# Kernel tuning notes

Measured on AMD Instinct MI355X. Metric: run time of the kernel, lower is better.

Reference implementation:

```python
import jax, jax.numpy as jnp
import numpy as np

B, N, H = 32, 2048, 128


def _lstm_step(c, h, x, Wi, Wh, b):
    # flax LSTMCell: gates i,f,g,o; sigmoid/sigmoid/tanh/sigmoid
    gates = x @ Wi + h @ Wh + b  # (B,N,4H)
    i, f, g, o = jnp.split(gates, 4, axis=-1)
    c_new = jax.nn.sigmoid(f) * c + jax.nn.sigmoid(i) * jnp.tanh(g)
    h_new = jax.nn.sigmoid(o) * jnp.tanh(c_new)
    return c_new, h_new


def setup_inputs() -> dict:
    key = jax.random.key(0)
    ks = jax.random.split(key, 24)
    f32 = jnp.float32
    inp = {}
    inp['node_embeddings'] = jax.random.normal(ks[0], (B, N, H), f32)
    for nm, k in zip(['hs_c0', 'hs_h0', 'hs_c1', 'hs_h1'], ks[1:5]):
        inp[nm] = jax.random.normal(k, (B, N, H), f32)
    ip = jax.random.uniform(ks[5], (B, N), f32)
    inp['instruction_pointer'] = ip / jnp.sum(ip, axis=-1, keepdims=True)
    inp['Wi0'] = jax.random.normal(ks[6], (H, 4 * H), f32) * 0.05
    inp['Wh0'] = jax.random.normal(ks[7], (H, 4 * H), f32) * 0.05
    inp['b0'] = jnp.zeros((4 * H,), f32)
    inp['Wi1'] = jax.random.normal(ks[8], (H, 4 * H), f32) * 0.05
    inp['Wh1'] = jax.random.normal(ks[9], (H, 4 * H), f32) * 0.05
    inp['b1'] = jnp.zeros((4 * H,), f32)
    inp['W_raise'] = jax.random.normal(ks[10], (4 * H, 2), f32) * 0.05
    inp['b_raise'] = jnp.zeros((2,), f32)
    inp['W_branch'] = jax.random.normal(ks[11], (4 * H, 2), f32) * 0.05
    inp['b_branch'] = jnp.zeros((2,), f32)
    inp['true_indexes'] = jax.random.randint(ks[12], (B, N), 0, N, jnp.int32)
    inp['false_indexes'] = jax.random.randint(ks[13], (B, N), 0, N, jnp.int32)
    inp['raise_indexes'] = jax.random.randint(ks[14], (B, N), 0, N, jnp.int32)
    inp['exit_node_indexes'] = jax.random.randint(ks[15], (B,), 0, N, jnp.int32)
    inp['raise_node_indexes'] = jax.random.randint(ks[16], (B,), 0, N, jnp.int32)
    inp['step_limits'] = jax.random.randint(ks[17], (B,), 0, 100, jnp.int32)
    inp['current_step'] = 5
    return inp


def reference(node_embeddings, hs_c0, hs_h0, hs_c1, hs_h1, instruction_pointer,
              Wi0, Wh0, b0, Wi1, Wh1, b1, W_raise, b_raise, W_branch, b_branch,
              true_indexes, false_indexes, raise_indexes,
              exit_node_indexes, raise_node_indexes, step_limits, current_step):
    bidx = jnp.arange(B)
    old = [hs_c0, hs_h0, hs_c1, hs_h1]

    # execute: per-node 2-layer stacked LSTM (vectorized over B,N)
    c0n, h0n = _lstm_step(hs_c0, hs_h0, node_embeddings, Wi0, Wh0, b0)
    c1n, h1n = _lstm_step(hs_c1, hs_h1, h0n, Wi1, Wh1, b1)
    contrib = [c0n, h0n, c1n, h1n]

    # mask_h: keep old state at exit node and (raise_in_ipagnn) at raise node
    def mask_nodes(hc, ho, idx):
        return hc.at[bidx, idx].set(ho[bidx, idx])
    contrib = [mask_nodes(mask_nodes(hc, ho, exit_node_indexes), ho, raise_node_indexes)
               for hc, ho in zip(contrib, old)]

    hs_emb = jnp.concatenate(contrib, axis=-1)  # (B,N,4H)

    raise_dec = jax.nn.softmax(hs_emb @ W_raise + b_raise, axis=-1)
    zero_one = jnp.array([0.0, 1.0], dtype=raise_dec.dtype)
    raise_dec = raise_dec.at[bidx, exit_node_indexes].set(zero_one)
    raise_dec = raise_dec.at[bidx, raise_node_indexes].set(zero_one)
    branch_dec = jax.nn.softmax(hs_emb @ W_branch + b_branch, axis=-1)

    p_raise = raise_dec[..., 0]
    p_noraise = raise_dec[..., 1]
    p_true = p_noraise * branch_dec[..., 0]
    p_false = p_noraise * branch_dec[..., 1]

    seg = jax.vmap(lambda v, idx: jax.ops.segment_sum(v, idx, num_segments=N))
    ip = instruction_pointer
    ip_new = (seg(p_raise * ip, raise_indexes)
              + seg(p_true * ip, true_indexes)
              + seg(p_false * ip, false_indexes))  # (B,N)
    denom = (ip_new + 1e-7)[..., None]

    wr = (p_raise * ip)[..., None]
    wt = (p_true * ip)[..., None]
    wf = (p_false * ip)[..., None]

    def agg(h):
        return (seg(h * wr, raise_indexes) + seg(h * wt, true_indexes)
                + seg(h * wf, false_indexes)) / denom
    hs_new = [agg(h) for h in contrib]

    # keep_old_if_done
    not_done = (current_step < step_limits)  # (B,)
    hs_out = [jnp.where(not_done[:, None, None], hn, ho) for hn, ho in zip(hs_new, old)]
    ip_out = jnp.where(not_done[:, None], ip_new, ip)

    # pack carry: (c0,h0,c1,h1, instruction_pointer) -> (B,N,4H+1)
    return jnp.concatenate(hs_out + [ip_out[..., None]], axis=-1)
```

## Files before the change

### kernel.cpp

```cpp
#include <hip/hip_runtime.h>
#include <stdint.h>

#define BB 32
#define NN 2048
#define HH 128
#define BN (BB*NN)

typedef short v8s __attribute__((ext_vector_type(8)));
typedef float v4f __attribute__((ext_vector_type(4)));

__device__ __forceinline__ unsigned short f2b(float f){
  union { float f; unsigned int i; } v; v.f = f;
  unsigned int x = v.i;
  unsigned int r = x + 0x7FFFu + ((x >> 16) & 1u);
  return (unsigned short)(r >> 16);
}
__device__ __forceinline__ unsigned int pk2(float a, float b){
  return (unsigned int)f2b(a) | ((unsigned int)f2b(b) << 16);
}
__device__ __forceinline__ float b2f(unsigned int s){
  union { unsigned int i; float f; } v; v.i = s << 16; return v.f;
}
__device__ __forceinline__ float frcp(float x){ return __builtin_amdgcn_rcpf(x); }
__device__ __forceinline__ float fsigm(float x){ return frcp(1.0f + __expf(-x)); }
__device__ __forceinline__ float ftanh(float x){ return 1.0f - 2.0f*frcp(1.0f + __expf(2.0f*x)); }

__global__ __launch_bounds__(1024) void kprep(
    const int* __restrict__ ri, const int* __restrict__ ti,
    const int* __restrict__ fi,
    int* __restrict__ counts, int* __restrict__ offsets,
    unsigned short* __restrict__ edges,
    const float* __restrict__ Wi0, const float* __restrict__ Wh0,
    const float* __restrict__ Wi1, const float* __restrict__ Wh1,
    unsigned short* __restrict__ Bsw0, unsigned short* __restrict__ Bsw1)
{
  __shared__ int cnt[NN];
  __shared__ int off[NN];
  __shared__ int cur[NN];
  __shared__ int wpart[16];

  int tid = threadIdx.x;

  if (blockIdx.x >= 32){
    int idx = (blockIdx.x - 32)*1024 + tid;
    int bid = idx >> 6;
    int lane = idx & 63;
    int layer = bid >> 8;
    int kc = (bid >> 5) & 7;
    int ct = bid & 31;
    const float* Wi = layer ? Wi1 : Wi0;
    const float* Wh = layer ? Wh1 : Wh0;
    unsigned short* dst = layer ? Bsw1 : Bsw0;
    int col = ct*16 + (lane & 15);
    int kbase = kc*32 + (lane >> 4)*8;
    size_t o = ((size_t)(kc*32 + ct)*64 + (size_t)lane)*8;
    #pragma unroll
    for (int j = 0; j < 8; j++){
      int k = kbase + j;
      dst[o + j] = f2b((k < 128) ? Wi[k*512 + col] : Wh[(k-128)*512 + col]);
    }
    return;
  }

  int b = blockIdx.x;
  const int* rp = ri + b*NN;
  const int* tp = ti + b*NN;
  const int* fp = fi + b*NN;

  #pragma unroll
  for (int p = 0; p < 2; p++){ cnt[p*1024 + tid] = 0; cur[p*1024 + tid] = 0; }
  __syncthreads();

  int rv[2], tv[2], fv[2];
  #pragma unroll
  for (int p = 0; p < 2; p++){
    int n = p*1024 + tid;
    rv[p] = rp[n]; tv[p] = tp[n]; fv[p] = fp[n];
    atomicAdd(&cnt[rv[p]], 1);
    atomicAdd(&cnt[tv[p]], 1);
    atomicAdd(&cnt[fv[p]], 1);
  }
  __syncthreads();

  int c0 = cnt[2*tid], c1 = cnt[2*tid+1];
  int s = c0 + c1;
  int lane = tid & 63, wv = tid >> 6;
  int inc = s;
  #pragma unroll
  for (int d = 1; d < 64; d <<= 1){
    int t = __shfl_up(inc, d, 64);
    if (lane >= d) inc += t;
  }
  if (lane == 63) wpart[wv] = inc;
  __syncthreads();
  if (tid == 0){
    int run = 0;
    #pragma unroll
    for (int w = 0; w < 16; w++){ int t = wpart[w]; wpart[w] = run; run += t; }
  }
  __syncthreads();
  int excl = wpart[wv] + inc - s;
  off[2*tid]   = excl;
  off[2*tid+1] = excl + c0;
  offsets[b*NN + 2*tid]   = excl;
  offsets[b*NN + 2*tid+1] = excl + c0;
  counts[b*NN + 2*tid]   = c0;
  counts[b*NN + 2*tid+1] = c1;
  __syncthreads();

  size_t ebase = (size_t)b*3*NN;
  #pragma unroll
  for (int p = 0; p < 2; p++){
    int n = p*1024 + tid;
    int t0 = rv[p]; int p0 = atomicAdd(&cur[t0], 1);
    edges[ebase + off[t0] + p0] = (unsigned short)n;
    int t1 = tv[p]; int p1 = atomicAdd(&cur[t1], 1);
    edges[ebase + off[t1] + p1] = (unsigned short)(n | (1<<11));
    int t2 = fv[p]; int p2 = atomicAdd(&cur[t2], 1);
    edges[ebase + off[t2] + p2] = (unsigned short)(n | (2<<11));
  }
}

#define ROWSB 32
#define PA 264
#define PH 136

__global__ __launch_bounds__(512, 4) void klstm2(
    const float* __restrict__ ne,
    float* __restrict__ c0, float* __restrict__ h0,
    float* __restrict__ c1, float* __restrict__ h1,
    unsigned short* __restrict__ sc0, unsigned short* __restrict__ sh0,
    unsigned short* __restrict__ sc1, unsigned short* __restrict__ sh1,
    const unsigned short* __restrict__ Bsw0, const float* __restrict__ b0,
    const unsigned short* __restrict__ Bsw1, const float* __restrict__ b1,
    const int* __restrict__ exit_idx, const int* __restrict__ raise_idx,
    const int* __restrict__ step_limits, const int* __restrict__ cur_step,
    int useb)
{
  __shared__ unsigned short ldsA[ROWSB*PA];
  __shared__ unsigned short ldsH[ROWSB*PH];
  __shared__ unsigned short ldsG[ROWSB*PH];

  int rowbase = blockIdx.x * ROWSB;
  int b = rowbase >> 11;
  if (cur_step[0] >= step_limits[b]) return;

  int tid = threadIdx.x;
  int wid = tid >> 6, lane = tid & 63;
  int quad = lane >> 4, l16 = lane & 15;
  int ch = wid*16 + l16;
  int e_row = exit_idx[b], r_row = raise_idx[b];

  #pragma unroll
  for (int p = 0; p < 4; p++){
    int idx = p*512 + tid;
    int row = idx >> 6, chunk = idx & 63;
    size_t g = (size_t)(rowbase + row)*128 + (chunk & 31)*4;
    float4 v = (chunk < 32) ? *(const float4*)(ne + g) : *(const float4*)(h0 + g);
    uint2 w; w.x = pk2(v.x, v.y); w.y = pk2(v.z, v.w);
    *(uint2*)&ldsA[row*PA + chunk*4] = w;
  }
  __syncthreads();

  float cpre[8], bias[4];
  #pragma unroll
  for (int rt = 0; rt < 2; rt++)
    #pragma unroll
    for (int r = 0; r < 4; r++)
      cpre[rt*4+r] = c0[((size_t)rowbase + rt*16 + quad*4 + r)*128 + ch];
  #pragma unroll
  for (int g = 0; g < 4; g++) bias[g] = b0[g*128 + ch];

  #pragma unroll
  for (int p = 0; p < 2; p++){
    int idx = p*512 + tid;
    int row = idx >> 5, chunk = idx & 31;
    float4 v = *(const float4*)(h1 + (size_t)(rowbase + row)*128 + chunk*4);
    uint2 w; w.x = pk2(v.x, v.y); w.y = pk2(v.z, v.w);
    *(uint2*)&ldsH[row*PH + chunk*4] = w;
  }

  const v8s* Bv0 = (const v8s*)Bsw0;
  v4f acc[2][4] = {};
  v8s bc[4], bn[4];
  #pragma unroll
  for (int g = 0; g < 4; g++) bc[g] = Bv0[(size_t)(g*8 + wid)*64 + lane];
  #pragma unroll
  for (int kc = 0; kc < 8; kc++){
    if (kc < 7){
      #pragma unroll
      for (int g = 0; g < 4; g++) bn[g] = Bv0[(size_t)((kc+1)*32 + g*8 + wid)*64 + lane];
    }
    v8s a0 = *(const v8s*)&ldsA[(0*16 + l16)*PA + kc*32 + quad*8];
    v8s a1 = *(const v8s*)&ldsA[(1*16 + l16)*PA + kc*32 + quad*8];
    #pragma unroll
    for (int g = 0; g < 4; g++){
      acc[0][g] = __builtin_amdgcn_mfma_f32_16x16x32_bf16(a0, bc[g], acc[0][g], 0,0,0);
      acc[1][g] = __builtin_amdgcn_mfma_f32_16x16x32_bf16(a1, bc[g], acc[1][g], 0,0,0);
    }
    #pragma unroll
    for (int g = 0; g < 4; g++) bc[g] = bn[g];
  }

  #pragma unroll
  for (int rt = 0; rt < 2; rt++){
    #pragma unroll
    for (int r = 0; r < 4; r++){
      int k = rt*4 + r;
      int lrow = rt*16 + quad*4 + r;
      int grow = rowbase + lrow;
      int node = grow & 2047;
      bool special = (node == e_row) || (node == r_row);
      float iv = acc[rt][0][r] + bias[0];
      float fv = acc[rt][1][r] + bias[1];
      float gv = acc[rt][2][r] + bias[2];
      float ov = acc[rt][3][r] + bias[3];
      float cn = fsigm(fv)*cpre[k] + fsigm(iv)*ftanh(gv);
      float hn = fsigm(ov)*ftanh(cn);
      if (useb){
        sc0[(size_t)grow*128 + ch] = special ? f2b(cpre[k]) : f2b(cn);
        sh0[(size_t)grow*128 + ch] = special ? ldsA[lrow*PA + 128 + ch] : f2b(hn);
      } else if (!special){
        c0[(size_t)grow*128 + ch] = cn;
        h0[(size_t)grow*128 + ch] = hn;
      }
      ldsG[lrow*PH + ch] = f2b(hn);
    }
  }

  #pragma unroll
  for (int rt = 0; rt < 2; rt++)
    #pragma unroll
    for (int r = 0; r < 4; r++)
      cpre[rt*4+r] = c1[((size_t)rowbase + rt*16 + quad*4 + r)*128 + ch];
  #pragma unroll
  for (int g = 0; g < 4; g++) bias[g] = b1[g*128 + ch];
  const v8s* Bv1 = (const v8s*)Bsw1;
  #pragma unroll
  for (int g = 0; g < 4; g++) bc[g] = Bv1[(size_t)(g*8 + wid)*64 + lane];

  __syncthreads();

  #pragma unroll
  for (int rt = 0; rt < 2; rt++)
    #pragma unroll
    for (int g = 0; g < 4; g++)
      acc[rt][g] = (v4f){0.f, 0.f, 0.f, 0.f};
  #pragma unroll
  for (int kc = 0; kc < 8; kc++){
    if (kc < 7){
      #pragma unroll
      for (int g = 0; g < 4; g++) bn[g] = Bv1[(size_t)((kc+1)*32 + g*8 + wid)*64 + lane];
    }
    v8s a0, a1;
    if (kc < 4){
      a0 = *(const v8s*)&ldsG[(0*16 + l16)*PH + kc*32 + quad*8];
      a1 = *(const v8s*)&ldsG[(1*16 + l16)*PH + kc*32 + quad*8];
    } else {
      a0 = *(const v8s*)&ldsH[(0*16 + l16)*PH + (kc-4)*32 + quad*8];
      a1 = *(const v8s*)&ldsH[(1*16 + l16)*PH + (kc-4)*32 + quad*8];
    }
    #pragma unroll
    for (int g = 0; g < 4; g++){
      acc[0][g] = __builtin_amdgcn_mfma_f32_16x16x32_bf16(a0, bc[g], acc[0][g], 0,0,0);
      acc[1][g] = __builtin_amdgcn_mfma_f32_16x16x32_bf16(a1, bc[g], acc[1][g], 0,0,0);
    }
    #pragma unroll
    for (int g = 0; g < 4; g++) bc[g] = bn[g];
  }

  #pragma unroll
  for (int rt = 0; rt < 2; rt++){
    #pragma unroll
    for (int r = 0; r < 4; r++){
      int k = rt*4 + r;
      int lrow = rt*16 + quad*4 + r;
      int grow = rowbase + lrow;
      int node = grow & 2047;
      bool special = (node == e_row) || (node == r_row);
      float iv = acc[rt][0][r] + bias[0];
      float fv = acc[rt][1][r] + bias[1];
      float gv = acc[rt][2][r] + bias[2];
      float ov = acc[rt][3][r] + bias[3];
      float cn = fsigm(fv)*cpre[k] + fsigm(iv)*ftanh(gv);
      float hn = fsigm(ov)*ftanh(cn);
      if (useb){
        sc1[(size_t)grow*128 + ch] = special ? f2b(cpre[k]) : f2b(cn);
        sh1[(size_t)grow*128 + ch] = special ? ldsH[lrow*PH + ch] : f2b(hn);
      } else if (!special){
        c1[(size_t)grow*128 + ch] = cn;
        h1[(size_t)grow*128 + ch] = hn;
      }
    }
  }
}

__global__ __launch_bounds__(256) void kdec(
    const float* __restrict__ c0, const float* __restrict__ h0,
    const float* __restrict__ c1, const float* __restrict__ h1,
    const unsigned short* __restrict__ sc0, const unsigned short* __restrict__ sh0,
    const unsigned short* __restrict__ sc1, const unsigned short* __restrict__ sh1,
    const float* __restrict__ Wr, const float* __restrict__ br,
    const float* __restrict__ Wb, const float* __restrict__ bb,
    const float* __restrict__ ip,
    const int* __restrict__ exit_idx, const int* __restrict__ raise_idx,
    float* __restrict__ wbuf, int useb)
{
  int tid = threadIdx.x;
  int wid = tid >> 6, lane = tid & 63;
  int gid = blockIdx.x*4 + wid;
  int b = gid >> 11, n = gid & 2047;

  float hv[8];
  if (useb){
    const unsigned short* bufs16[4] = {sc0, sh0, sc1, sh1};
    const unsigned short* hb = bufs16[lane >> 4] + (size_t)gid*128 + (lane & 15)*8;
    uint4 raw = *(const uint4*)hb;
    hv[0] = b2f(raw.x & 0xffffu); hv[1] = b2f(raw.x >> 16);
    hv[2] = b2f(raw.y & 0xffffu); hv[3] = b2f(raw.y >> 16);
    hv[4] = b2f(raw.z & 0xffffu); hv[5] = b2f(raw.z >> 16);
    hv[6] = b2f(raw.w & 0xffffu); hv[7] = b2f(raw.w >> 16);
  } else {
    const float* bufs[4] = {c0, h0, c1, h1};
    const float* hb = bufs[lane >> 4] + (size_t)gid*128 + (lane & 15)*8;
    float4 hv0 = *(const float4*)hb;
    float4 hv1 = *(const float4*)(hb + 4);
    hv[0]=hv0.x; hv[1]=hv0.y; hv[2]=hv0.z; hv[3]=hv0.w;
    hv[4]=hv1.x; hv[5]=hv1.y; hv[6]=hv1.z; hv[7]=hv1.w;
  }
  const float* wrp = Wr + lane*16;
  const float* wbp = Wb + lane*16;
  float r0=0.f, r1=0.f, q0=0.f, q1=0.f;
  #pragma unroll
  for (int j = 0; j < 8; j++){
    float h = hv[j];
    r0 += h * wrp[j*2];  r1 += h * wrp[j*2+1];
    q0 += h * wbp[j*2];  q1 += h * wbp[j*2+1];
  }
  #pragma unroll
  for (int off = 32; off > 0; off >>= 1){
    r0 += __shfl_xor(r0, off, 64);
    r1 += __shfl_xor(r1, off, 64);
    q0 += __shfl_xor(q0, off, 64);
    q1 += __shfl_xor(q1, off, 64);
  }
  if (lane == 0){
    r0 += br[0]; r1 += br[1];
    q0 += bb[0]; q1 += bb[1];
    float pr, pn;
    if (n == exit_idx[b] || n == raise_idx[b]){ pr = 0.f; pn = 1.f; }
    else {
      float m = fmaxf(r0, r1);
      float e0 = __expf(r0 - m), e1 = __expf(r1 - m);
      pr = e0 / (e0 + e1); pn = e1 / (e0 + e1);
    }
    float m2 = fmaxf(q0, q1);
    float f0 = __expf(q0 - m2), f1 = __expf(q1 - m2);
    float pt = f0 / (f0 + f1), pf = f1 / (f0 + f1);
    float ipv = ip[gid];
    wbuf[0*BN + gid] = pr * ipv;
    wbuf[1*BN + gid] = pn * pt * ipv;
    wbuf[2*BN + gid] = pn * pf * ipv;
  }
}

__global__ __launch_bounds__(512) void kagg(
    const float* __restrict__ c0, const float* __restrict__ h0,
    const float* __restrict__ c1, const float* __restrict__ h1,
    const unsigned short* __restrict__ sc0, const unsigned short* __restrict__ sh0,
    const unsigned short* __restrict__ sc1, const unsigned short* __restrict__ sh1,
    const float* __restrict__ ip,
    const float* __restrict__ wbuf, const unsigned short* __restrict__ edges,
    const int* __restrict__ counts, const int* __restrict__ offsets,
    const int* __restrict__ step_limits, const int* __restrict__ cur_step,
    float* __restrict__ out, int useb)
{
  int tid0 = threadIdx.x;
  int sub = tid0 >> 7;
  int tid = tid0 & 127;
  int gid = blockIdx.x*4 + sub;
  int b = gid >> 11;
  size_t obase = (size_t)gid*513;
  const float* bufs[4] = {c0, h0, c1, h1};

  if (cur_step[0] >= step_limits[b]){
    int c = tid*4;
    const float* s = bufs[c >> 7];
    size_t rb = (size_t)gid*128 + (c & 127);
    out[obase + c+0] = s[rb+0];
    out[obase + c+1] = s[rb+1];
    out[obase + c+2] = s[rb+2];
    out[obase + c+3] = s[rb+3];
    if (tid == 0) out[obase + 512] = ip[gid];
    return;
  }

  int cnt = counts[gid], off = offsets[gid];
  const unsigned short* eb = edges + (size_t)b*3*NN + off;
  int lane = tid & 63;
  int coff = (tid & 31)*4;
  float a0=0.f, a1=0.f, a2=0.f, a3=0.f, ipn=0.f;

  if (useb){
    const unsigned short* bufs16[4] = {sc0, sh0, sc1, sh1};
    const unsigned short* sb = bufs16[tid >> 5];
    for (int base = 0; base < cnt; base += 64){
      int e = base + lane;
      int n_l = 0; float w_l = 0.f;
      if (e < cnt){
        int pk = eb[e];
        n_l = pk & 2047;
        w_l = wbuf[(pk >> 11)*BN + (b<<11) + n_l];
      }
      int m = min(cnt - base, 64);
      for (int j = 0; j < m; j++){
        int   n = __shfl(n_l, j, 64);
        float w = __shfl(w_l, j, 64);
        uint2 raw = *(const uint2*)(sb + ((size_t)(b<<11) + n)*128 + coff);
        ipn += w;
        a0 += w * b2f(raw.x & 0xffffu);
        a1 += w * b2f(raw.x >> 16);
        a2 += w * b2f(raw.y & 0xffffu);
        a3 += w * b2f(raw.y >> 16);
      }
    }
  } else {
    const float* sb = bufs[tid >> 5];
    for (int base = 0; base < cnt; base += 64){
      int e = base + lane;
      int n_l = 0; float w_l = 0.f;
      if (e < cnt){
        int pk = eb[e];
        n_l = pk & 2047;
        w_l = wbuf[(pk >> 11)*BN + (b<<11) + n_l];
      }
      int m = min(cnt - base, 64);
      for (int j = 0; j < m; j++){
        int   n = __shfl(n_l, j, 64);
        float w = __shfl(w_l, j, 64);
        float4 sv = *(const float4*)(sb + ((size_t)(b<<11) + n)*128 + coff);
        ipn += w;
        a0 += w * sv.x;
        a1 += w * sv.y;
        a2 += w * sv.z;
        a3 += w * sv.w;
      }
    }
  }
  int c = tid*4;
  float inv = 1.0f / (ipn + 1e-7f);
  out[obase + c+0] = a0*inv;
  out[obase + c+1] = a1*inv;
  out[obase + c+2] = a2*inv;
  out[obase + c+3] = a3*inv;
  if (tid == 0) out[obase + 512] = ipn;
}

extern "C" void kernel_launch(void* const* d_in, const int* in_sizes, int n_in,
                              void* d_out, int out_size, void* d_ws, size_t ws_size,
                              hipStream_t stream){
  const float* ne  = (const float*)d_in[0];
  float* c0  = (float*)d_in[1];
  float* h0  = (float*)d_in[2];
  float* c1  = (float*)d_in[3];
  float* h1  = (float*)d_in[4];
  const float* ip  = (const float*)d_in[5];
  const float* Wi0 = (const float*)d_in[6];
  const float* Wh0 = (const float*)d_in[7];
  const float* b0  = (const float*)d_in[8];
  const float* Wi1 = (const float*)d_in[9];
  const float* Wh1 = (const float*)d_in[10];
  const float* b1  = (const float*)d_in[11];
  const float* Wr  = (const float*)d_in[12];
  const float* br  = (const float*)d_in[13];
  const float* Wb  = (const float*)d_in[14];
  const float* bb  = (const float*)d_in[15];
  const int* ti  = (const int*)d_in[16];
  const int* fi  = (const int*)d_in[17];
  const int* ri  = (const int*)d_in[18];
  const int* ei  = (const int*)d_in[19];
  const int* rni = (const int*)d_in[20];
  const int* sl  = (const int*)d_in[21];
  const int* cs  = (const int*)d_in[22];
  float* out = (float*)d_out;

  uint8_t* ws = (uint8_t*)d_ws;
  unsigned short* Bsw0    = (unsigned short*)(ws + 0);
  unsigned short* Bsw1    = (unsigned short*)(ws + 262144);
  float*          wbuf    = (float*)(ws + 655360);
  int*            counts  = (int*)(ws + 1441792);
  int*            offsets = (int*)(ws + 1703936);
  unsigned short* edges   = (unsigned short*)(ws + 2228224);
  const size_t SBASE = 2621440;
  const size_t SB    = (size_t)BN * 128 * 2;
  int useb = (ws_size >= SBASE + 4*SB) ? 1 : 0;
  unsigned short* sc0 = (unsigned short*)(ws + SBASE + 0*SB);
  unsigned short* sh0 = (unsigned short*)(ws + SBASE + 1*SB);
  unsigned short* sc1 = (unsigned short*)(ws + SBASE + 2*SB);
  unsigned short* sh1 = (unsigned short*)(ws + SBASE + 3*SB);

  kprep<<<64, 1024, 0, stream>>>(ri, ti, fi, counts, offsets, edges,
                                 Wi0, Wh0, Wi1, Wh1, Bsw0, Bsw1);

  klstm2<<<BN/ROWSB, 512, 0, stream>>>(ne, c0, h0, c1, h1,
                                       sc0, sh0, sc1, sh1,
                                       Bsw0, b0, Bsw1, b1,
                                       ei, rni, sl, cs, useb);

  kdec<<<BN/4, 256, 0, stream>>>(c0, h0, c1, h1, sc0, sh0, sc1, sh1,
                                 Wr, br, Wb, bb, ip, ei, rni, wbuf, useb);

  kagg<<<BN/4, 512, 0, stream>>>(c0, h0, c1, h1, sc0, sh0, sc1, sh1,
                                 ip, wbuf, edges, counts, offsets,
                                 sl, cs, out, useb);
}
```

Before: 424.5 us.

## Fold CSR edge-list build into LSTM kernel and use nontemporal output stores

The CSR construction (counts, offsets, edges) moves out of the prep kernel and runs in 32 extra blocks of the LSTM kernel, so it overlaps with the LSTM GEMM work. It uses a union of LDS structs so both roles share shared memory. The prep kernel now only swizzles the weights into bf16 with a 512-thread launch. Output stores in the aggregation kernel become nontemporal to avoid polluting the cache. The CSR blocks now have 512 threads handling 4 nodes each, and the union may raise the LDS footprint of LSTM blocks, which could affect occupancy.

```diff
diff --git a/kernel.cpp b/kernel.cpp
--- a/kernel.cpp
+++ b/kernel.cpp
@@ -25,105 +25,44 @@
 __device__ __forceinline__ float fsigm(float x){ return frcp(1.0f + __expf(-x)); }
 __device__ __forceinline__ float ftanh(float x){ return 1.0f - 2.0f*frcp(1.0f + __expf(2.0f*x)); }
 
-__global__ __launch_bounds__(1024) void kprep(
-    const int* __restrict__ ri, const int* __restrict__ ti,
-    const int* __restrict__ fi,
-    int* __restrict__ counts, int* __restrict__ offsets,
-    unsigned short* __restrict__ edges,
+__global__ __launch_bounds__(512) void kswz(
     const float* __restrict__ Wi0, const float* __restrict__ Wh0,
     const float* __restrict__ Wi1, const float* __restrict__ Wh1,
-    unsigned short* __restrict__ Bsw0, unsigned short* __restrict__ Bsw1)
-{
-  __shared__ int cnt[NN];
-  __shared__ int off[NN];
-  __shared__ int cur[NN];
-  __shared__ int wpart[16];
-
-  int tid = threadIdx.x;
-
-  if (blockIdx.x >= 32){
-    int idx = (blockIdx.x - 32)*1024 + tid;
-    int bid = idx >> 6;
-    int lane = idx & 63;
-    int layer = bid >> 8;
-    int kc = (bid >> 5) & 7;
-    int ct = bid & 31;
-    const float* Wi = layer ? Wi1 : Wi0;
-    const float* Wh = layer ? Wh1 : Wh0;
-    unsigned short* dst = layer ? Bsw1 : Bsw0;
-    int col = ct*16 + (lane & 15);
-    int kbase = kc*32 + (lane >> 4)*8;
-    size_t o = ((size_t)(kc*32 + ct)*64 + (size_t)lane)*8;
-    #pragma unroll
-    for (int j = 0; j < 8; j++){
-      int k = kbase + j;
-      dst[o + j] = f2b((k < 128) ? Wi[k*512 + col] : Wh[(k-128)*512 + col]);
-    }
-    return;
-  }
-
-  int b = blockIdx.x;
-  const int* rp = ri + b*NN;
-  const int* tp = ti + b*NN;
-  const int* fp = fi + b*NN;
-
-  #pragma unroll
-  for (int p = 0; p < 2; p++){ cnt[p*1024 + tid] = 0; cur[p*1024 + tid] = 0; }
-  __syncthreads();
-
-  int rv[2], tv[2], fv[2];
-  #pragma unroll
-  for (int p = 0; p < 2; p++){
-    int n = p*1024 + tid;
-    rv[p] = rp[n]; tv[p] = tp[n]; fv[p] = fp[n];
-    atomicAdd(&cnt[rv[p]], 1);
-    atomicAdd(&cnt[tv[p]], 1);
-    atomicAdd(&cnt[fv[p]], 1);
-  }
-  __syncthreads();
-
-  int c0 = cnt[2*tid], c1 = cnt[2*tid+1];
-  int s = c0 + c1;
-  int lane = tid & 63, wv = tid >> 6;
-  int inc = s;
-  #pragma unroll
-  for (int d = 1; d < 64; d <<= 1){
-    int t = __shfl_up(inc, d, 64);
-    if (lane >= d) inc += t;
-  }
-  if (lane == 63) wpart[wv] = inc;
-  __syncthreads();
-  if (tid == 0){
-    int run = 0;
-    #pragma unroll
-    for (int w = 0; w < 16; w++){ int t = wpart[w]; wpart[w] = run; run += t; }
-  }
-  __syncthreads();
-  int excl = wpart[wv] + inc - s;
-  off[2*tid]   = excl;
-  off[2*tid+1] = excl + c0;
-  offsets[b*NN + 2*tid]   = excl;
-  offsets[b*NN + 2*tid+1] = excl + c0;
-  counts[b*NN + 2*tid]   = c0;
-  counts[b*NN + 2*tid+1] = c1;
-  __syncthreads();
-
-  size_t ebase = (size_t)b*3*NN;
-  #pragma unroll
-  for (int p = 0; p < 2; p++){
-    int n = p*1024 + tid;
-    int t0 = rv[p]; int p0 = atomicAdd(&cur[t0], 1);
-    edges[ebase + off[t0] + p0] = (unsigned short)n;
-    int t1 = tv[p]; int p1 = atomicAdd(&cur[t1], 1);
-    edges[ebase + off[t1] + p1] = (unsigned short)(n | (1<<11));
-    int t2 = fv[p]; int p2 = atomicAdd(&cur[t2], 1);
-    edges[ebase + off[t2] + p2] = (unsigned short)(n | (2<<11));
+    unsigned short* __restrict__ Bsw0, unsigned short* __restrict__ Bsw1){
+  int idx = blockIdx.x*512 + threadIdx.x;
+  int bid = idx >> 6;
+  int lane = idx & 63;
+  int layer = bid >> 8;
+  int kc = (bid >> 5) & 7;
+  int ct = bid & 31;
+  const float* Wi = layer ? Wi1 : Wi0;
+  const float* Wh = layer ? Wh1 : Wh0;
+  unsigned short* dst = layer ? Bsw1 : Bsw0;
+  int col = ct*16 + (lane & 15);
+  int kbase = kc*32 + (lane >> 4)*8;
+  size_t o = ((size_t)(kc*32 + ct)*64 + (size_t)lane)*8;
+  #pragma unroll
+  for (int j = 0; j < 8; j++){
+    int k = kbase + j;
+    dst[o + j] = f2b((k < 128) ? Wi[k*512 + col] : Wh[(k-128)*512 + col]);
   }
 }
 
 #define ROWSB 32
 #define PA 264
 #define PH 136
+
+struct LstmLds {
+  unsigned short A[ROWSB*PA];
+  unsigned short H[ROWSB*PH];
+  unsigned short G[ROWSB*PH];
+};
+struct CsrLds {
+  int cnt[NN];
+  int off[NN];
+  int cur[NN];
+  int wpart[8];
+};
 
 __global__ __launch_bounds__(512, 4) void klstm2(
     const float* __restrict__ ne,
@@ -134,18 +73,89 @@
     const unsigned short* __restrict__ Bsw0, const float* __restrict__ b0,
     const unsigned short* __restrict__ Bsw1, const float* __restrict__ b1,
     const int* __restrict__ exit_idx, const int* __restrict__ raise_idx,
+    const int* __restrict__ ri, const int* __restrict__ ti,
+    const int* __restrict__ fi,
+    int* __restrict__ counts, int* __restrict__ offsets,
+    unsigned short* __restrict__ edges,
     const int* __restrict__ step_limits, const int* __restrict__ cur_step,
     int useb)
 {
-  __shared__ unsigned short ldsA[ROWSB*PA];
-  __shared__ unsigned short ldsH[ROWSB*PH];
-  __shared__ unsigned short ldsG[ROWSB*PH];
-
-  int rowbase = blockIdx.x * ROWSB;
+  __shared__ union { LstmLds l; CsrLds c; } u;
+
+  int tid = threadIdx.x;
+
+  if (blockIdx.x < 32){
+    int b = blockIdx.x;
+    const int* rp = ri + b*NN;
+    const int* tp = ti + b*NN;
+    const int* fp = fi + b*NN;
+
+    #pragma unroll
+    for (int p = 0; p < 4; p++){ u.c.cnt[p*512 + tid] = 0; u.c.cur[p*512 + tid] = 0; }
+    __syncthreads();
+
+    int rv[4], tv[4], fv[4];
+    #pragma unroll
+    for (int p = 0; p < 4; p++){
+      int n = p*512 + tid;
+      rv[p] = rp[n]; tv[p] = tp[n]; fv[p] = fp[n];
+      atomicAdd(&u.c.cnt[rv[p]], 1);
+      atomicAdd(&u.c.cnt[tv[p]], 1);
+      atomicAdd(&u.c.cnt[fv[p]], 1);
+    }
+    __syncthreads();
+
+    int cc0 = u.c.cnt[4*tid], cc1 = u.c.cnt[4*tid+1];
+    int cc2 = u.c.cnt[4*tid+2], cc3 = u.c.cnt[4*tid+3];
+    int s = cc0 + cc1 + cc2 + cc3;
+    int lane = tid & 63, wv = tid >> 6;
+    int inc = s;
+    #pragma unroll
+    for (int d = 1; d < 64; d <<= 1){
+      int t = __shfl_up(inc, d, 64);
+      if (lane >= d) inc += t;
+    }
+    if (lane == 63) u.c.wpart[wv] = inc;
+    __syncthreads();
+    if (tid == 0){
+      int run = 0;
+      #pragma unroll
+      for (int w = 0; w < 8; w++){ int t = u.c.wpart[w]; u.c.wpart[w] = run; run += t; }
+    }
+    __syncthreads();
+    int excl = u.c.wpart[wv] + inc - s;
+    u.c.off[4*tid]   = excl;
+    u.c.off[4*tid+1] = excl + cc0;
+    u.c.off[4*tid+2] = excl + cc0 + cc1;
+    u.c.off[4*tid+3] = excl + cc0 + cc1 + cc2;
+    offsets[b*NN + 4*tid]   = excl;
+    offsets[b*NN + 4*tid+1] = excl + cc0;
+    offsets[b*NN + 4*tid+2] = excl + cc0 + cc1;
+    offsets[b*NN + 4*tid+3] = excl + cc0 + cc1 + cc2;
+    counts[b*NN + 4*tid]   = cc0;
+    counts[b*NN + 4*tid+1] = cc1;
+    counts[b*NN + 4*tid+2] = cc2;
+    counts[b*NN + 4*tid+3] = cc3;
+    __syncthreads();
+
+    size_t ebase = (size_t)b*3*NN;
+    #pragma unroll
+    for (int p = 0; p < 4; p++){
+      int n = p*512 + tid;
+      int t0 = rv[p]; int p0 = atomicAdd(&u.c.cur[t0], 1);
+      edges[ebase + u.c.off[t0] + p0] = (unsigned short)n;
+      int t1 = tv[p]; int p1 = atomicAdd(&u.c.cur[t1], 1);
+      edges[ebase + u.c.off[t1] + p1] = (unsigned short)(n | (1<<11));
+      int t2 = fv[p]; int p2 = atomicAdd(&u.c.cur[t2], 1);
+      edges[ebase + u.c.off[t2] + p2] = (unsigned short)(n | (2<<11));
+    }
+    return;
+  }
+
+  int rowbase = (blockIdx.x - 32) * ROWSB;
   int b = rowbase >> 11;
   if (cur_step[0] >= step_limits[b]) return;
 
-  int tid = threadIdx.x;
   int wid = tid >> 6, lane = tid & 63;
   int quad = lane >> 4, l16 = lane & 15;
   int ch = wid*16 + l16;
@@ -158,7 +168,7 @@
     size_t g = (size_t)(rowbase + row)*128 + (chunk & 31)*4;
     float4 v = (chunk < 32) ? *(const float4*)(ne + g) : *(const float4*)(h0 + g);
     uint2 w; w.x = pk2(v.x, v.y); w.y = pk2(v.z, v.w);
-    *(uint2*)&ldsA[row*PA + chunk*4] = w;
+    *(uint2*)&u.l.A[row*PA + chunk*4] = w;
   }
   __syncthreads();
 
@@ -177,7 +187,7 @@
     int row = idx >> 5, chunk = idx & 31;
     float4 v = *(const float4*)(h1 + (size_t)(rowbase + row)*128 + chunk*4);
     uint2 w; w.x = pk2(v.x, v.y); w.y = pk2(v.z, v.w);
-    *(uint2*)&ldsH[row*PH + chunk*4] = w;
+    *(uint2*)&u.l.H[row*PH + chunk*4] = w;
   }
 
   const v8s* Bv0 = (const v8s*)Bsw0;
@@ -191,8 +201,8 @@
       #pragma unroll
       for (int g = 0; g < 4; g++) bn[g] = Bv0[(size_t)((kc+1)*32 + g*8 + wid)*64 + lane];
     }
-    v8s a0 = *(const v8s*)&ldsA[(0*16 + l16)*PA + kc*32 + quad*8];
-    v8s a1 = *(const v8s*)&ldsA[(1*16 + l16)*PA + kc*32 + quad*8];
+    v8s a0 = *(const v8s*)&u.l.A[(0*16 + l16)*PA + kc*32 + quad*8];
+    v8s a1 = *(const v8s*)&u.l.A[(1*16 + l16)*PA + kc*32 + quad*8];
     #pragma unroll
     for (int g = 0; g < 4; g++){
       acc[0][g] = __builtin_amdgcn_mfma_f32_16x16x32_bf16(a0, bc[g], acc[0][g], 0,0,0);
@@ -219,12 +229,12 @@
       float hn = fsigm(ov)*ftanh(cn);
       if (useb){
         sc0[(size_t)grow*128 + ch] = special ? f2b(cpre[k]) : f2b(cn);
-        sh0[(size_t)grow*128 + ch] = special ? ldsA[lrow*PA + 128 + ch] : f2b(hn);
+        sh0[(size_t)grow*128 + ch] = special ? u.l.A[lrow*PA + 128 + ch] : f2b(hn);
       } else if (!special){
         c0[(size_t)grow*128 + ch] = cn;
         h0[(size_t)grow*128 + ch] = hn;
       }
-      ldsG[lrow*PH + ch] = f2b(hn);
+      u.l.G[lrow*PH + ch] = f2b(hn);
     }
   }
 
@@ -254,11 +264,11 @@
     }
     v8s a0, a1;
     if (kc < 4){
-      a0 = *(const v8s*)&ldsG[(0*16 + l16)*PH + kc*32 + quad*8];
-      a1 = *(const v8s*)&ldsG[(1*16 + l16)*PH + kc*32 + quad*8];
+      a0 = *(const v8s*)&u.l.G[(0*16 + l16)*PH + kc*32 + quad*8];
+      a1 = *(const v8s*)&u.l.G[(1*16 + l16)*PH + kc*32 + quad*8];
     } else {
-      a0 = *(const v8s*)&ldsH[(0*16 + l16)*PH + (kc-4)*32 + quad*8];
-      a1 = *(const v8s*)&ldsH[(1*16 + l16)*PH + (kc-4)*32 + quad*8];
+      a0 = *(const v8s*)&u.l.H[(0*16 + l16)*PH + (kc-4)*32 + quad*8];
+      a1 = *(const v8s*)&u.l.H[(1*16 + l16)*PH + (kc-4)*32 + quad*8];
     }
     #pragma unroll
     for (int g = 0; g < 4; g++){
@@ -286,7 +296,7 @@
       float hn = fsigm(ov)*ftanh(cn);
       if (useb){
         sc1[(size_t)grow*128 + ch] = special ? f2b(cpre[k]) : f2b(cn);
-        sh1[(size_t)grow*128 + ch] = special ? ldsH[lrow*PH + ch] : f2b(hn);
+        sh1[(size_t)grow*128 + ch] = special ? u.l.H[lrow*PH + ch] : f2b(hn);
       } else if (!special){
         c1[(size_t)grow*128 + ch] = cn;
         h1[(size_t)grow*128 + ch] = hn;
@@ -387,11 +397,11 @@
     int c = tid*4;
     const float* s = bufs[c >> 7];
     size_t rb = (size_t)gid*128 + (c & 127);
-    out[obase + c+0] = s[rb+0];
-    out[obase + c+1] = s[rb+1];
-    out[obase + c+2] = s[rb+2];
-    out[obase + c+3] = s[rb+3];
-    if (tid == 0) out[obase + 512] = ip[gid];
+    __builtin_nontemporal_store(s[rb+0], &out[obase + c+0]);
+    __builtin_nontemporal_store(s[rb+1], &out[obase + c+1]);
+    __builtin_nontemporal_store(s[rb+2], &out[obase + c+2]);
+    __builtin_nontemporal_store(s[rb+3], &out[obase + c+3]);
+    if (tid == 0) __builtin_nontemporal_store(ip[gid], &out[obase + 512]);
     return;
   }
 
@@ -449,11 +459,11 @@
   }
   int c = tid*4;
   float inv = 1.0f / (ipn + 1e-7f);
-  out[obase + c+0] = a0*inv;
-  out[obase + c+1] = a1*inv;
-  out[obase + c+2] = a2*inv;
-  out[obase + c+3] = a3*inv;
-  if (tid == 0) out[obase + 512] = ipn;
+  __builtin_nontemporal_store(a0*inv, &out[obase + c+0]);
+  __builtin_nontemporal_store(a1*inv, &out[obase + c+1]);
+  __builtin_nontemporal_store(a2*inv, &out[obase + c+2]);
+  __builtin_nontemporal_store(a3*inv, &out[obase + c+3]);
+  if (tid == 0) __builtin_nontemporal_store(ipn, &out[obase + 512]);
 }
 
 extern "C" void kernel_launch(void* const* d_in, const int* in_sizes, int n_in,
@@ -499,13 +509,14 @@
   unsigned short* sc1 = (unsigned short*)(ws + SBASE + 2*SB);
   unsigned short* sh1 = (unsigned short*)(ws + SBASE + 3*SB);
 
-  kprep<<<64, 1024, 0, stream>>>(ri, ti, fi, counts, offsets, edges,
-                                 Wi0, Wh0, Wi1, Wh1, Bsw0, Bsw1);
-
-  klstm2<<<BN/ROWSB, 512, 0, stream>>>(ne, c0, h0, c1, h1,
-                                       sc0, sh0, sc1, sh1,
-                                       Bsw0, b0, Bsw1, b1,
-                                       ei, rni, sl, cs, useb);
+  kswz<<<64, 512, 0, stream>>>(Wi0, Wh0, Wi1, Wh1, Bsw0, Bsw1);
+
+  klstm2<<<32 + BN/ROWSB, 512, 0, stream>>>(ne, c0, h0, c1, h1,
+                                            sc0, sh0, sc1, sh1,
+                                            Bsw0, b0, Bsw1, b1,
+                                            ei, rni, ri, ti, fi,
+                                            counts, offsets, edges,
+                                            sl, cs, useb);
 
   kdec<<<BN/4, 256, 0, stream>>>(c0, h0, c1, h1, sc0, sh0, sc1, sh1,
                                  Wr, br, Wb, bb, ip, ei, rni, wbuf, useb);
```

After: 419.2 us. Within noise of the previous version (-1.3%).
